# Kernel optimization log

Measured on AMD Instinct MI355X. Metric: run time of the kernel, lower is better.

## Reference

```python
import jax, jax.numpy as jnp
import numpy as np

N, E, IN, K, F, D = 50000, 800000, 256, 4, 64, 2


def setup_inputs() -> dict:
    key = jax.random.key(0)
    ks = jax.random.split(key, 10)
    # CSR rowptr: 0 .. E, nondecreasing, endpoints pinned
    inner = jnp.sort(jax.random.randint(ks[0], (N - 1,), 0, E + 1))
    rowptr = jnp.concatenate([jnp.zeros(1, jnp.int64), inner.astype(jnp.int64), jnp.full(1, E, jnp.int64)])
    colind = jax.random.randint(ks[1], (E,), 0, N).astype(jnp.int64)
    # CSC mirrors (used only by the fused kernel's backward; inert in forward math)
    inner_c = jnp.sort(jax.random.randint(ks[2], (N - 1,), 0, E + 1))
    colptr = jnp.concatenate([jnp.zeros(1, jnp.int64), inner_c.astype(jnp.int64), jnp.full(1, E, jnp.int64)])
    rowind = jax.random.randint(ks[3], (E,), 0, N).astype(jnp.int64)
    permute = jnp.arange(E, dtype=jnp.int64)
    feat = jax.random.normal(ks[4], (N, IN), dtype=jnp.float32)
    pseudo = jax.random.uniform(ks[5], (E, D), dtype=jnp.float32)
    # params: fc weight [K*F, IN] (xavier-normal style scale), mu ~ N(0, 0.1), inv_sigma = 1, bias = 0
    gain = float(np.sqrt(2.0))
    std = gain * float(np.sqrt(2.0 / (IN + K * F)))
    W_fc = jax.random.normal(ks[6], (K * F, IN), dtype=jnp.float32) * std
    mu = jax.random.normal(ks[7], (K, D), dtype=jnp.float32) * 0.1
    inv_sigma = jnp.ones((K, D), dtype=jnp.float32)
    bias = jnp.zeros((F,), dtype=jnp.float32)
    return {"rowptr": rowptr, "colind": colind, "colptr": colptr, "rowind": rowind,
            "permute": permute, "feat": feat, "pseudo": pseudo,
            "W_fc": W_fc, "mu": mu, "inv_sigma": inv_sigma, "bias": bias}


def reference(rowptr, colind, colptr, rowind, permute, feat, pseudo, W_fc, mu, inv_sigma, bias):
    n = feat.shape[0]
    e = colind.shape[0]
    k, d = mu.shape
    f = W_fc.shape[0] // k
    # dense projection: [N, K, F]
    node_feat = (feat @ W_fc.T).reshape(n, k, f)
    # per-edge Gaussian mixture weights: [E, K]
    diff = pseudo[:, None, :] - mu[None, :, :]              # [E, K, D]
    gaussian = jnp.exp(jnp.sum(-0.5 * diff * diff * (inv_sigma[None, :, :] ** 2), axis=-1))
    # multi-head SpMM: gather source feats, weight per kernel, sum kernels (sum commutes
    # with the segment reduction, so fold the head-sum into the edge message): [E, F]
    msg = jnp.einsum('ek,ekf->ef', gaussian, node_feat[colind])
    # destination node of each CSR edge
    dst = jnp.searchsorted(rowptr, jnp.arange(e), side='right') - 1
    rst = jax.ops.segment_sum(msg, dst, num_segments=n)      # [N, F]
    return rst + bias
```

## Files before the change

### kernel.cpp

```cpp
#include <hip/hip_runtime.h>


typedef __attribute__((ext_vector_type(8))) short bf16x8;
typedef __attribute__((ext_vector_type(4))) float f32x4;

__device__ inline unsigned short f32_to_bf16(float f) {
    union { float f; unsigned int u; } c; c.f = f;
    unsigned int u = c.u;
    u += 0x7fffu + ((u >> 16) & 1u);
    return (unsigned short)(u >> 16);
}
__device__ inline float bf16_to_f32(unsigned short h) {
    union { unsigned int u; float f; } c; c.u = ((unsigned int)h) << 16;
    return c.f;
}

#define LDST 40

__global__ __launch_bounds__(256, 2) void gemm_mfma(
    const float* __restrict__ A,
    const float* __restrict__ W,
    unsigned short* __restrict__ C,
    int M)
{
    __shared__ unsigned short As[128 * LDST];
    __shared__ unsigned short Bs[128 * LDST];
    const int t    = threadIdx.x;
    const int lane = t & 63;
    const int wave = t >> 6;
    const int wm   = (wave >> 1) * 64;
    const int wn   = (wave & 1) * 64;
    const int bm   = blockIdx.x * 128;
    const int bn   = blockIdx.y * 128;
    const int l16  = lane & 15;
    const int quad = lane >> 4;

    f32x4 acc[4][4];
#pragma unroll
    for (int mi = 0; mi < 4; ++mi)
#pragma unroll
        for (int ni = 0; ni < 4; ++ni)
            acc[mi][ni] = (f32x4){0.f, 0.f, 0.f, 0.f};

    for (int k0 = 0; k0 < 256; k0 += 32) {
#pragma unroll
        for (int i = 0; i < 4; ++i) {
            const int flat = (i * 256 + t) * 4;
            const int row  = flat >> 5;
            const int off  = flat & 31;
            const int grow = bm + row;
            float4 av = make_float4(0.f, 0.f, 0.f, 0.f);
            if (grow < M)
                av = *reinterpret_cast<const float4*>(A + (size_t)grow * 256 + k0 + off);
            const int jp   = bn + row;
            const int wrow = ((jp & 3) << 6) | (jp >> 2);
            const float4 wv = *reinterpret_cast<const float4*>(W + (size_t)wrow * 256 + k0 + off);
            ushort4 ah, wh;
            ah.x = f32_to_bf16(av.x); ah.y = f32_to_bf16(av.y);
            ah.z = f32_to_bf16(av.z); ah.w = f32_to_bf16(av.w);
            wh.x = f32_to_bf16(wv.x); wh.y = f32_to_bf16(wv.y);
            wh.z = f32_to_bf16(wv.z); wh.w = f32_to_bf16(wv.w);
            *reinterpret_cast<ushort4*>(&As[row * LDST + off]) = ah;
            *reinterpret_cast<ushort4*>(&Bs[row * LDST + off]) = wh;
        }
        __syncthreads();

        bf16x8 af[4], bfr[4];
#pragma unroll
        for (int mi = 0; mi < 4; ++mi)
            af[mi] = *reinterpret_cast<const bf16x8*>(&As[(wm + mi * 16 + l16) * LDST + quad * 8]);
#pragma unroll
        for (int ni = 0; ni < 4; ++ni)
            bfr[ni] = *reinterpret_cast<const bf16x8*>(&Bs[(wn + ni * 16 + l16) * LDST + quad * 8]);
#pragma unroll
        for (int mi = 0; mi < 4; ++mi)
#pragma unroll
            for (int ni = 0; ni < 4; ++ni)
                acc[mi][ni] = __builtin_amdgcn_mfma_f32_16x16x32_bf16(
                    af[mi], bfr[ni], acc[mi][ni], 0, 0, 0);
        __syncthreads();
    }

#pragma unroll
    for (int mi = 0; mi < 4; ++mi) {
#pragma unroll
        for (int r = 0; r < 4; ++r) {
            const int row = bm + wm + mi * 16 + quad * 4 + r;
            if (row < M) {
#pragma unroll
                for (int ni = 0; ni < 4; ++ni) {
                    const int col = bn + wn + ni * 16 + l16;
                    C[(size_t)row * 256 + col] = f32_to_bf16(acc[mi][ni][r]);
                }
            }
        }
    }
}

__global__ __launch_bounds__(256) void edge_aggregate(
    const int* __restrict__ rowptr,
    const int* __restrict__ colind,
    const float* __restrict__ pseudo,
    const unsigned short* __restrict__ nf,
    const float* __restrict__ mu,
    const float* __restrict__ inv_sigma,
    const float* __restrict__ bias,
    float* __restrict__ out,
    int N)
{
    __shared__ float gbuf[4][64];
    __shared__ int   cbuf[4][16];
    const int wave = threadIdx.x >> 6;
    const int lane = threadIdx.x & 63;
    const int node = blockIdx.x * 4 + wave;
    if (node >= N) return;

    const int kk = lane >> 4;
    const int ii = lane & 15;
    const float mx = mu[2 * kk], my = mu[2 * kk + 1];
    const float sa = inv_sigma[2 * kk], sb = inv_sigma[2 * kk + 1];
    const float sx = sa * sa, sy = sb * sb;

    const int e0 = rowptr[node];
    const int e1 = rowptr[node + 1];

    float* gw = gbuf[wave];
    int*   cw = cbuf[wave];

    float acc = 0.f;
    for (int ec = e0; ec < e1; ec += 16) {
        const int cnt = min(16, e1 - ec);
        if (ii < cnt) {
            const int e = ec + ii;
            const float2 p = *reinterpret_cast<const float2*>(pseudo + 2 * (size_t)e);
            const float dx = p.x - mx, dy = p.y - my;
            gw[ii * 4 + kk] = __expf(-0.5f * (dx * dx * sx + dy * dy * sy));
            if (kk == 0) cw[ii] = colind[e];
        }
        __builtin_amdgcn_wave_barrier();
        __threadfence_block();
        for (int i2 = 0; i2 < cnt; ++i2) {
            const int col = cw[i2];
            const float4 g = *reinterpret_cast<const float4*>(&gw[i2 * 4]);
            const ushort4 h = *reinterpret_cast<const ushort4*>(
                nf + ((size_t)col << 8) + (lane << 2));
            acc += g.x * bf16_to_f32(h.x) + g.y * bf16_to_f32(h.y)
                 + g.z * bf16_to_f32(h.z) + g.w * bf16_to_f32(h.w);
        }
        __builtin_amdgcn_wave_barrier();
        __threadfence_block();
    }
    out[((size_t)node << 6) + lane] = acc + bias[lane];
}

extern "C" void kernel_launch(void* const* d_in, const int* in_sizes, int n_in,
                              void* d_out, int out_size, void* d_ws, size_t ws_size,
                              hipStream_t stream)
{
    const int*   rowptr    = (const int*)d_in[0];
    const int*   colind    = (const int*)d_in[1];
    const float* feat      = (const float*)d_in[5];
    const float* pseudo    = (const float*)d_in[6];
    const float* W_fc      = (const float*)d_in[7];
    const float* mu        = (const float*)d_in[8];
    const float* inv_sigma = (const float*)d_in[9];
    const float* bias      = (const float*)d_in[10];
    float* out = (float*)d_out;
    unsigned short* nf = (unsigned short*)d_ws;

    const int N = in_sizes[0] - 1;

    dim3 gGemm((N + 127) / 128, 2);
    hipLaunchKernelGGL(gemm_mfma, gGemm, dim3(256), 0, stream, feat, W_fc, nf, N);

    const int blocks = (N + 3) / 4;
    hipLaunchKernelGGL(edge_aggregate, dim3(blocks), dim3(256), 0, stream,
                       rowptr, colind, pseudo, nf, mu, inv_sigma, bias, out, N);
}
```

Before: 202.6 us.

## Pre-convert W to bf16 and load GEMM operands directly from global memory

```diff
diff --git a/kernel.cpp b/kernel.cpp
--- a/kernel.cpp
+++ b/kernel.cpp
@@ -15,23 +15,35 @@
     return c.f;
 }
 
-#define LDST 40
-
-__global__ __launch_bounds__(256, 2) void gemm_mfma(
+__global__ __launch_bounds__(256) void convert_W(
+    const float* __restrict__ W, unsigned short* __restrict__ Wp)
+{
+    const int t = blockIdx.x * 256 + threadIdx.x;
+#pragma unroll
+    for (int r = 0; r < 2; ++r) {
+        const int fi = t + r * 8192;
+        const int jp = fi >> 6;
+        const int k4 = fi & 63;
+        const int wrow = ((jp & 3) << 6) | (jp >> 2);
+        const float4 v = reinterpret_cast<const float4*>(W)[wrow * 64 + k4];
+        ushort4 h;
+        h.x = f32_to_bf16(v.x); h.y = f32_to_bf16(v.y);
+        h.z = f32_to_bf16(v.z); h.w = f32_to_bf16(v.w);
+        reinterpret_cast<ushort4*>(Wp)[jp * 64 + k4] = h;
+    }
+}
+
+__global__ __launch_bounds__(256) void gemm_direct(
     const float* __restrict__ A,
-    const float* __restrict__ W,
+    const unsigned short* __restrict__ Wp,
     unsigned short* __restrict__ C,
     int M)
 {
-    __shared__ unsigned short As[128 * LDST];
-    __shared__ unsigned short Bs[128 * LDST];
     const int t    = threadIdx.x;
     const int lane = t & 63;
     const int wave = t >> 6;
-    const int wm   = (wave >> 1) * 64;
-    const int wn   = (wave & 1) * 64;
-    const int bm   = blockIdx.x * 128;
-    const int bn   = blockIdx.y * 128;
+    const int wn   = wave * 64;
+    const int bm   = blockIdx.x * 64;
     const int l16  = lane & 15;
     const int quad = lane >> 4;
 
@@ -42,54 +54,49 @@
         for (int ni = 0; ni < 4; ++ni)
             acc[mi][ni] = (f32x4){0.f, 0.f, 0.f, 0.f};
 
+    int arow[4];
+#pragma unroll
+    for (int mi = 0; mi < 4; ++mi) {
+        int r = bm + mi * 16 + l16;
+        arow[mi] = r < M ? r : (M - 1);
+    }
+
+#pragma unroll 2
     for (int k0 = 0; k0 < 256; k0 += 32) {
-#pragma unroll
-        for (int i = 0; i < 4; ++i) {
-            const int flat = (i * 256 + t) * 4;
-            const int row  = flat >> 5;
-            const int off  = flat & 31;
-            const int grow = bm + row;
-            float4 av = make_float4(0.f, 0.f, 0.f, 0.f);
-            if (grow < M)
-                av = *reinterpret_cast<const float4*>(A + (size_t)grow * 256 + k0 + off);
-            const int jp   = bn + row;
-            const int wrow = ((jp & 3) << 6) | (jp >> 2);
-            const float4 wv = *reinterpret_cast<const float4*>(W + (size_t)wrow * 256 + k0 + off);
-            ushort4 ah, wh;
-            ah.x = f32_to_bf16(av.x); ah.y = f32_to_bf16(av.y);
-            ah.z = f32_to_bf16(av.z); ah.w = f32_to_bf16(av.w);
-            wh.x = f32_to_bf16(wv.x); wh.y = f32_to_bf16(wv.y);
-            wh.z = f32_to_bf16(wv.z); wh.w = f32_to_bf16(wv.w);
-            *reinterpret_cast<ushort4*>(&As[row * LDST + off]) = ah;
-            *reinterpret_cast<ushort4*>(&Bs[row * LDST + off]) = wh;
-        }
-        __syncthreads();
-
         bf16x8 af[4], bfr[4];
 #pragma unroll
-        for (int mi = 0; mi < 4; ++mi)
-            af[mi] = *reinterpret_cast<const bf16x8*>(&As[(wm + mi * 16 + l16) * LDST + quad * 8]);
-#pragma unroll
         for (int ni = 0; ni < 4; ++ni)
-            bfr[ni] = *reinterpret_cast<const bf16x8*>(&Bs[(wn + ni * 16 + l16) * LDST + quad * 8]);
+            bfr[ni] = *reinterpret_cast<const bf16x8*>(
+                Wp + (size_t)(wn + ni * 16 + l16) * 256 + k0 + quad * 8);
+#pragma unroll
+        for (int mi = 0; mi < 4; ++mi) {
+            const float* p = A + (size_t)arow[mi] * 256 + k0 + quad * 8;
+            const float4 a0 = *reinterpret_cast<const float4*>(p);
+            const float4 a1 = *reinterpret_cast<const float4*>(p + 4);
+            union { bf16x8 v; unsigned short s[8]; } pk;
+            pk.s[0] = f32_to_bf16(a0.x); pk.s[1] = f32_to_bf16(a0.y);
+            pk.s[2] = f32_to_bf16(a0.z); pk.s[3] = f32_to_bf16(a0.w);
+            pk.s[4] = f32_to_bf16(a1.x); pk.s[5] = f32_to_bf16(a1.y);
+            pk.s[6] = f32_to_bf16(a1.z); pk.s[7] = f32_to_bf16(a1.w);
+            af[mi] = pk.v;
+        }
 #pragma unroll
         for (int mi = 0; mi < 4; ++mi)
 #pragma unroll
             for (int ni = 0; ni < 4; ++ni)
                 acc[mi][ni] = __builtin_amdgcn_mfma_f32_16x16x32_bf16(
                     af[mi], bfr[ni], acc[mi][ni], 0, 0, 0);
-        __syncthreads();
     }
 
 #pragma unroll
     for (int mi = 0; mi < 4; ++mi) {
 #pragma unroll
         for (int r = 0; r < 4; ++r) {
-            const int row = bm + wm + mi * 16 + quad * 4 + r;
+            const int row = bm + mi * 16 + quad * 4 + r;
             if (row < M) {
 #pragma unroll
                 for (int ni = 0; ni < 4; ++ni) {
-                    const int col = bn + wn + ni * 16 + l16;
+                    const int col = wn + ni * 16 + l16;
                     C[(size_t)row * 256 + col] = f32_to_bf16(acc[mi][ni][r]);
                 }
             }
@@ -139,13 +146,25 @@
         }
         __builtin_amdgcn_wave_barrier();
         __threadfence_block();
-        for (int i2 = 0; i2 < cnt; ++i2) {
-            const int col = cw[i2];
-            const float4 g = *reinterpret_cast<const float4*>(&gw[i2 * 4]);
-            const ushort4 h = *reinterpret_cast<const ushort4*>(
-                nf + ((size_t)col << 8) + (lane << 2));
-            acc += g.x * bf16_to_f32(h.x) + g.y * bf16_to_f32(h.y)
-                 + g.z * bf16_to_f32(h.z) + g.w * bf16_to_f32(h.w);
+        if (cnt == 16) {
+#pragma unroll
+            for (int i2 = 0; i2 < 16; ++i2) {
+                const int col = cw[i2];
+                const float4 g = *reinterpret_cast<const float4*>(&gw[i2 * 4]);
+                const ushort4 h = *reinterpret_cast<const ushort4*>(
+                    nf + ((size_t)col << 8) + (lane << 2));
+                acc += g.x * bf16_to_f32(h.x) + g.y * bf16_to_f32(h.y)
+                     + g.z * bf16_to_f32(h.z) + g.w * bf16_to_f32(h.w);
+            }
+        } else {
+            for (int i2 = 0; i2 < cnt; ++i2) {
+                const int col = cw[i2];
+                const float4 g = *reinterpret_cast<const float4*>(&gw[i2 * 4]);
+                const ushort4 h = *reinterpret_cast<const ushort4*>(
+                    nf + ((size_t)col << 8) + (lane << 2));
+                acc += g.x * bf16_to_f32(h.x) + g.y * bf16_to_f32(h.y)
+                     + g.z * bf16_to_f32(h.z) + g.w * bf16_to_f32(h.w);
+            }
         }
         __builtin_amdgcn_wave_barrier();
         __threadfence_block();
@@ -167,11 +186,14 @@
     const float* bias      = (const float*)d_in[10];
     float* out = (float*)d_out;
     unsigned short* nf = (unsigned short*)d_ws;
+    unsigned short* Wp = (unsigned short*)d_out;
 
     const int N = in_sizes[0] - 1;
 
-    dim3 gGemm((N + 127) / 128, 2);
-    hipLaunchKernelGGL(gemm_mfma, gGemm, dim3(256), 0, stream, feat, W_fc, nf, N);
+    hipLaunchKernelGGL(convert_W, dim3(32), dim3(256), 0, stream, W_fc, Wp);
+
+    const int gBlocks = (N + 63) / 64;
+    hipLaunchKernelGGL(gemm_direct, dim3(gBlocks), dim3(256), 0, stream, feat, Wp, nf, N);
 
     const int blocks = (N + 3) / 4;
     hipLaunchKernelGGL(edge_aggregate, dim3(blocks), dim3(256), 0, stream,
```

New measurement: 232.3 us. 14.7% more time.

## Pre-convert GEMM inputs to bf16 and stream tiles via global_load_lds

Applied to the files above, without the earlier changes.

```diff
diff --git a/kernel.cpp b/kernel.cpp
--- a/kernel.cpp
+++ b/kernel.cpp
@@ -14,14 +14,115 @@
     union { unsigned int u; float f; } c; c.u = ((unsigned int)h) << 16;
     return c.f;
 }
-
-#define LDST 40
-
-__global__ __launch_bounds__(256, 2) void gemm_mfma(
-    const float* __restrict__ A,
-    const float* __restrict__ W,
+__device__ inline ushort4 cvt4(float4 v) {
+    ushort4 h;
+    h.x = f32_to_bf16(v.x); h.y = f32_to_bf16(v.y);
+    h.z = f32_to_bf16(v.z); h.w = f32_to_bf16(v.w);
+    return h;
+}
+
+__global__ __launch_bounds__(256) void convert_inputs(
+    const float* __restrict__ W, const float* __restrict__ feat,
+    unsigned short* __restrict__ Wp, unsigned short* __restrict__ Af,
+    int nFeat4)
+{
+    const int gid = blockIdx.x * 256 + threadIdx.x;
+    if (gid < 16384) {
+        const int jp = gid >> 6, k4 = gid & 63;
+        const int wrow = ((jp & 3) << 6) | (jp >> 2);
+        reinterpret_cast<ushort4*>(Wp)[jp * 64 + k4] =
+            cvt4(reinterpret_cast<const float4*>(W)[wrow * 64 + k4]);
+    }
+    for (int i = gid; i < nFeat4; i += gridDim.x * 256)
+        reinterpret_cast<ushort4*>(Af)[i] =
+            cvt4(reinterpret_cast<const float4*>(feat)[i]);
+}
+
+__global__ void gemm_lds(
+    const unsigned short* __restrict__ Af,
+    const unsigned short* __restrict__ Wp,
     unsigned short* __restrict__ C,
     int M)
+{
+    __shared__ unsigned short As[128 * 32];
+    __shared__ unsigned short Bs[128 * 32];
+    const int t    = threadIdx.x;
+    const int lane = t & 63;
+    const int wave = t >> 6;
+    const int bn   = blockIdx.x * 128;
+    const int bm   = blockIdx.y * 128;
+    const int l16  = lane & 15;
+    const int quad = lane >> 4;
+    const int wm   = (wave >> 1) * 64;
+    const int wn   = (wave & 1) * 64;
+
+    const int r0 = wave * 32 + (lane >> 2);
+    const int r1 = r0 + 16;
+    const int kc = (lane & 3) * 8;
+    const size_t ar0 = (size_t)min(bm + r0, M - 1) * 256 + kc;
+    const size_t ar1 = (size_t)min(bm + r1, M - 1) * 256 + kc;
+    const size_t br0 = (size_t)(bn + r0) * 256 + kc;
+    const size_t br1 = (size_t)(bn + r1) * 256 + kc;
+
+    f32x4 acc[4][4];
+#pragma unroll
+    for (int mi = 0; mi < 4; ++mi)
+#pragma unroll
+        for (int ni = 0; ni < 4; ++ni)
+            acc[mi][ni] = (f32x4){0.f, 0.f, 0.f, 0.f};
+
+    typedef __attribute__((address_space(3))) void lds_t;
+    typedef const __attribute__((address_space(1))) void gm_t;
+
+    for (int k0 = 0; k0 < 256; k0 += 32) {
+        __builtin_amdgcn_global_load_lds((gm_t*)(Af + ar0 + k0),
+            (lds_t*)(As + wave * 1024), 16, 0, 0);
+        __builtin_amdgcn_global_load_lds((gm_t*)(Af + ar1 + k0),
+            (lds_t*)(As + wave * 1024 + 512), 16, 0, 0);
+        __builtin_amdgcn_global_load_lds((gm_t*)(Wp + br0 + k0),
+            (lds_t*)(Bs + wave * 1024), 16, 0, 0);
+        __builtin_amdgcn_global_load_lds((gm_t*)(Wp + br1 + k0),
+            (lds_t*)(Bs + wave * 1024 + 512), 16, 0, 0);
+        __syncthreads();
+
+        bf16x8 af[4], bfr[4];
+#pragma unroll
+        for (int mi = 0; mi < 4; ++mi)
+            af[mi] = *reinterpret_cast<const bf16x8*>(
+                &As[(wm + mi * 16 + l16) * 32 + quad * 8]);
+#pragma unroll
+        for (int ni = 0; ni < 4; ++ni)
+            bfr[ni] = *reinterpret_cast<const bf16x8*>(
+                &Bs[(wn + ni * 16 + l16) * 32 + quad * 8]);
+#pragma unroll
+        for (int mi = 0; mi < 4; ++mi)
+#pragma unroll
+            for (int ni = 0; ni < 4; ++ni)
+                acc[mi][ni] = __builtin_amdgcn_mfma_f32_16x16x32_bf16(
+                    af[mi], bfr[ni], acc[mi][ni], 0, 0, 0);
+        __syncthreads();
+    }
+
+#pragma unroll
+    for (int mi = 0; mi < 4; ++mi) {
+#pragma unroll
+        for (int r = 0; r < 4; ++r) {
+            const int row = bm + wm + mi * 16 + quad * 4 + r;
+            if (row < M) {
+#pragma unroll
+                for (int ni = 0; ni < 4; ++ni) {
+                    const int col = bn + wn + ni * 16 + l16;
+                    C[(size_t)row * 256 + col] = f32_to_bf16(acc[mi][ni][r]);
+                }
+            }
+        }
+    }
+}
+
+#define LDST 40
+__global__ __launch_bounds__(256, 2) void gemm_fallback(
+    const float* __restrict__ A, const float* __restrict__ W,
+    unsigned short* __restrict__ C, int M)
 {
     __shared__ unsigned short As[128 * LDST];
     __shared__ unsigned short Bs[128 * LDST];
@@ -55,16 +156,10 @@
             const int jp   = bn + row;
             const int wrow = ((jp & 3) << 6) | (jp >> 2);
             const float4 wv = *reinterpret_cast<const float4*>(W + (size_t)wrow * 256 + k0 + off);
-            ushort4 ah, wh;
-            ah.x = f32_to_bf16(av.x); ah.y = f32_to_bf16(av.y);
-            ah.z = f32_to_bf16(av.z); ah.w = f32_to_bf16(av.w);
-            wh.x = f32_to_bf16(wv.x); wh.y = f32_to_bf16(wv.y);
-            wh.z = f32_to_bf16(wv.z); wh.w = f32_to_bf16(wv.w);
-            *reinterpret_cast<ushort4*>(&As[row * LDST + off]) = ah;
-            *reinterpret_cast<ushort4*>(&Bs[row * LDST + off]) = wh;
-        }
-        __syncthreads();
-
+            *reinterpret_cast<ushort4*>(&As[row * LDST + off]) = cvt4(av);
+            *reinterpret_cast<ushort4*>(&Bs[row * LDST + off]) = cvt4(wv);
+        }
+        __syncthreads();
         bf16x8 af[4], bfr[4];
 #pragma unroll
         for (int mi = 0; mi < 4; ++mi)
@@ -80,7 +175,6 @@
                     af[mi], bfr[ni], acc[mi][ni], 0, 0, 0);
         __syncthreads();
     }
-
 #pragma unroll
     for (int mi = 0; mi < 4; ++mi) {
 #pragma unroll
@@ -123,7 +217,6 @@
 
     const int e0 = rowptr[node];
     const int e1 = rowptr[node + 1];
-
     float* gw = gbuf[wave];
     int*   cw = cbuf[wave];
 
@@ -166,14 +259,23 @@
     const float* inv_sigma = (const float*)d_in[9];
     const float* bias      = (const float*)d_in[10];
     float* out = (float*)d_out;
+
+    const int N = in_sizes[0] - 1;
     unsigned short* nf = (unsigned short*)d_ws;
-
-    const int N = in_sizes[0] - 1;
-
-    dim3 gGemm((N + 127) / 128, 2);
-    hipLaunchKernelGGL(gemm_mfma, gGemm, dim3(256), 0, stream, feat, W_fc, nf, N);
-
-    const int blocks = (N + 3) / 4;
-    hipLaunchKernelGGL(edge_aggregate, dim3(blocks), dim3(256), 0, stream,
+    const size_t nfElems = (size_t)N * 256;
+
+    if (ws_size >= nfElems * 4) {
+        unsigned short* Af = nf + nfElems;
+        unsigned short* Wp = (unsigned short*)d_out;
+        hipLaunchKernelGGL(convert_inputs, dim3(1024), dim3(256), 0, stream,
+                           W_fc, feat, Wp, Af, N * 64);
+        hipLaunchKernelGGL(gemm_lds, dim3(2, (N + 127) / 128), dim3(256), 0, stream,
+                           Af, Wp, nf, N);
+    } else {
+        hipLaunchKernelGGL(gemm_fallback, dim3((N + 127) / 128, 2), dim3(256), 0,
+                           stream, feat, W_fc, nf, N);
+    }
+
+    hipLaunchKernelGGL(edge_aggregate, dim3((N + 3) / 4), dim3(256), 0, stream,
                        rowptr, colind, pseudo, nf, mu, inv_sigma, bias, out, N);
 }
```

Measured after the change: 198.6 us. 1.02x faster.
